# Performance work log

Measured on AMD Instinct MI355X. Metric: run time of the kernel, lower is better.

## Reference

```python
import jax, jax.numpy as jnp
import numpy as np

N = 100000
E = 1600000
D_IN, D_HID, D_OUT = 128, 128, 128


def gcn_conv(x, edge_index, W, b):
    """PyG GCNConv with default symmetric normalization and added self-loops.
    out = D^{-1/2} (A + I) D^{-1/2} (x W) + b, edge weights = 1.
    """
    n = x.shape[0]
    h = x @ W                                   # [N, D_out]
    src, dst = edge_index[0], edge_index[1]     # messages flow src -> dst
    ones = jnp.ones(src.shape[0], dtype=x.dtype)
    # degree includes the self-loop (+1), computed on the target index as in PyG
    deg = jax.ops.segment_sum(ones, dst, num_segments=n) + 1.0  # [N]
    dinv = jax.lax.rsqrt(deg)                   # deg >= 1 so safe
    norm = dinv[src] * dinv[dst]                # [E]
    msg = h[src] * norm[:, None]                # [E, D_out]
    agg = jax.ops.segment_sum(msg, dst, num_segments=n)
    # self-loop contribution: norm = dinv_i * dinv_i = 1/deg_i
    out = agg + h * (dinv * dinv)[:, None] + b
    return out


def layer_norm(x, gamma, beta, eps=1e-5):
    mu = jnp.mean(x, axis=-1, keepdims=True)
    var = jnp.mean(jnp.square(x - mu), axis=-1, keepdims=True)
    return (x - mu) * jax.lax.rsqrt(var + eps) * gamma + beta


def setup_inputs() -> dict:
    key = jax.random.key(0)
    ks = jax.random.split(key, 8)
    x = jax.random.normal(ks[0], (N, D_IN), dtype=jnp.float32)
    edge_index = jax.random.randint(ks[1], (2, E), 0, N, dtype=jnp.int64)
    s1 = 1.0 / np.sqrt(D_IN)
    s2 = 1.0 / np.sqrt(D_HID)
    W1 = jax.random.uniform(ks[2], (D_IN, D_HID), jnp.float32, -s1, s1)
    b1 = jnp.zeros((D_HID,), jnp.float32)
    W2 = jax.random.uniform(ks[3], (D_HID, D_OUT), jnp.float32, -s2, s2)
    b2 = jnp.zeros((D_OUT,), jnp.float32)
    gamma = jnp.ones((D_OUT,), jnp.float32)
    beta = jnp.zeros((D_OUT,), jnp.float32)
    return {"x": x, "edge_index": edge_index, "W1": W1, "b1": b1,
            "W2": W2, "b2": b2, "gamma": gamma, "beta": beta}


def reference(x, edge_index, W1, b1, W2, b2, gamma, beta):
    h = gcn_conv(x, edge_index, W1, b1)
    h = jax.nn.relu(h)
    # dropout is identity in eval mode (deterministic reference)
    h = gcn_conv(h, edge_index, W2, b2)
    return layer_norm(h, gamma, beta)
```

## Files before the change

kernel.cpp:

```cpp
#include <hip/hip_runtime.h>


#define N_NODES 100000
#define N_EDGES 1600000
#define NBLK_N  391
#define NB      196
#define BKT_CAP 8960
#define BIN_GRID 391
#define GEMM_GRID 1563

typedef unsigned int  u32;
typedef unsigned short u16;
typedef __attribute__((ext_vector_type(8))) short bf16x8;
typedef __attribute__((ext_vector_type(4))) float f32x4;

__device__ __forceinline__ float bflo(u32 u){ return __uint_as_float(u << 16); }
__device__ __forceinline__ float bfhi(u32 u){ return __uint_as_float(u & 0xFFFF0000u); }
__device__ __forceinline__ u32 f2b(float f){
  u32 u = __float_as_uint(f);
  return (u + 0x7FFFu + ((u >> 16) & 1u)) >> 16;
}
__device__ __forceinline__ u32 pack2(float a, float b){ return f2b(a) | (f2b(b) << 16); }
__device__ __forceinline__ u32 clampN(int s){
  u32 u = (u32)s;
  return (u < (u32)N_NODES) ? u : (u32)(N_NODES - 1);
}

__global__ __launch_bounds__(64) void detect(const int* __restrict__ ei,
                                             int* __restrict__ flags){
  int l = threadIdx.x;
  int nzodd = (ei[2 * l + 1] != 0) ? 1 : 0;
  #pragma unroll
  for (int o = 32; o > 0; o >>= 1) nzodd += __shfl_xor(nzodd, o, 64);
  if (l == 0) flags[1] = (nzodd == 0) ? 1 : 0;
}


__device__ __forceinline__ void build_wfrag(u16* wfrag, const float* __restrict__ W,
                                            int tid){
  #pragma unroll
  for (int i = 0; i < 8; ++i){
    int fid   = tid + i * 256;
    int lane  = fid & 63;
    int kb    = (fid >> 6) & 3;
    int ntile = fid >> 8;
    int n  = ntile * 16 + (lane & 15);
    int k0 = kb * 32 + (lane >> 4) * 8;
    u16 tmp[8];
    #pragma unroll
    for (int j = 0; j < 8; ++j) tmp[j] = (u16)f2b(W[(k0 + j) * 128 + n]);
    *(bf16x8*)(wfrag + (size_t)fid * 8) = *(const bf16x8*)tmp;
  }
}

__device__ __forceinline__ void gemm_tail(const u16* wfrag, const bf16x8 afrag[4],
                                          int rowbase, int lane, u16* __restrict__ Hout,
                                          int nrows){
  const int m = lane & 15, q = lane >> 4;
  f32x4 acc[8];
  #pragma unroll
  for (int n = 0; n < 8; ++n) acc[n] = (f32x4){0.f, 0.f, 0.f, 0.f};
  #pragma unroll
  for (int n = 0; n < 8; ++n){
    #pragma unroll
    for (int kb = 0; kb < 4; ++kb){
      bf16x8 bfrag = *(const bf16x8*)(wfrag + ((size_t)(n * 4 + kb) * 64 + lane) * 8);
      acc[n] = __builtin_amdgcn_mfma_f32_16x16x32_bf16(afrag[kb], bfrag, acc[n], 0, 0, 0);
    }
  }
  #pragma unroll
  for (int r = 0; r < 4; ++r){
    int orow = rowbase + q * 4 + r;
    if (orow < nrows){
      u16* Or = Hout + (size_t)orow * 128 + m;
      #pragma unroll
      for (int n = 0; n < 8; ++n) Or[n * 16] = (u16)f2b(acc[n][r]);
    }
  }
}

__device__ __forceinline__ void gemm_f32_body(u16* wfrag, const float* __restrict__ A,
                                              const float* __restrict__ W,
                                              u16* __restrict__ Hout, int nrows, int bid){
  build_wfrag(wfrag, W, threadIdx.x);
  __syncthreads();
  const int lane = threadIdx.x & 63;
  const int wv   = threadIdx.x >> 6;
  const int rowbase = bid * 64 + wv * 16;
  const int row  = rowbase + (lane & 15);
  const int rowc = (row < nrows) ? row : (nrows - 1);
  const int q    = lane >> 4;
  bf16x8 afrag[4];
  const float* Ar = A + (size_t)rowc * 128;
  #pragma unroll
  for (int kb = 0; kb < 4; ++kb){
    f32x4 p0 = *(const f32x4*)(Ar + kb * 32 + q * 8);
    f32x4 p1 = *(const f32x4*)(Ar + kb * 32 + q * 8 + 4);
    bf16x8 f;
    f[0] = (short)f2b(p0[0]); f[1] = (short)f2b(p0[1]);
    f[2] = (short)f2b(p0[2]); f[3] = (short)f2b(p0[3]);
    f[4] = (short)f2b(p1[0]); f[5] = (short)f2b(p1[1]);
    f[6] = (short)f2b(p1[2]); f[7] = (short)f2b(p1[3]);
    afrag[kb] = f;
  }
  gemm_tail(wfrag, afrag, rowbase, lane, Hout, nrows);
}

__device__ __forceinline__ void gemm_bf16_body(u16* wfrag, const u16* __restrict__ A,
                                               const float* __restrict__ W,
                                               u16* __restrict__ Hout, int nrows, int bid){
  build_wfrag(wfrag, W, threadIdx.x);
  __syncthreads();
  const int lane = threadIdx.x & 63;
  const int wv   = threadIdx.x >> 6;
  const int rowbase = bid * 64 + wv * 16;
  const int row  = rowbase + (lane & 15);
  const int rowc = (row < nrows) ? row : (nrows - 1);
  const int q    = lane >> 4;
  bf16x8 afrag[4];
  const u16* Ar = A + (size_t)rowc * 128;
  #pragma unroll
  for (int kb = 0; kb < 4; ++kb)
    afrag[kb] = *(const bf16x8*)(Ar + kb * 32 + q * 8);
  gemm_tail(wfrag, afrag, rowbase, lane, Hout, nrows);
}


__device__ __forceinline__ void binA_body(u32* cnt ,
                                          const int* __restrict__ ei,
                                          const int* __restrict__ flags,
                                          u32* __restrict__ binned,
                                          u32* __restrict__ bucket_fill, int bb){
  u32* gbase = cnt + 256;
  const int tid = threadIdx.x;
  cnt[tid] = 0;
  __syncthreads();
  const int i64  = flags[1];
  const int base = bb * 4096;
  u32 pk[16], rk[16], bk[16];
  #pragma unroll
  for (int j = 0; j < 16; ++j){
    int e = base + tid + j * 256;
    bk[j] = 0xFFFFFFFFu;
    if (e < N_EDGES){
      int dsti = i64 ? ei[2 * N_EDGES + 2 * e] : ei[N_EDGES + e];
      int srci = i64 ? ei[2 * e]               : ei[e];
      u32 ud = clampN(dsti), us = clampN(srci);
      u32 b = ud >> 9;
      bk[j] = b;
      pk[j] = us | ((ud & 511u) << 17);
      rk[j] = atomicAdd(&cnt[b], 1u);
    }
  }
  __syncthreads();
  u32 c = cnt[tid];
  u32 old = 0;
  if (c) old = atomicAdd(&bucket_fill[tid < NB ? tid : 0], tid < NB ? c : 0u);
  gbase[tid] = old;
  __syncthreads();
  #pragma unroll
  for (int j = 0; j < 16; ++j){
    if (bk[j] != 0xFFFFFFFFu){
      u32 idx = gbase[bk[j]] + rk[j];
      if (idx < BKT_CAP) binned[(size_t)bk[j] * BKT_CAP + idx] = pk[j];
    }
  }
}


__global__ __launch_bounds__(256) void fused_gemm_bin(const float* __restrict__ A,
                                                      const float* __restrict__ W,
                                                      u16* __restrict__ Hout,
                                                      const int* __restrict__ ei,
                                                      const int* __restrict__ flags,
                                                      u32* __restrict__ binned,
                                                      u32* __restrict__ bucket_fill){
  __shared__ u16 smem[16384];
  if (blockIdx.x < GEMM_GRID){
    gemm_f32_body(smem, A, W, Hout, N_NODES, blockIdx.x);
  } else {
    binA_body((u32*)smem, ei, flags, binned, bucket_fill, blockIdx.x - GEMM_GRID);
  }
}

__global__ __launch_bounds__(256) void gemm_f32in(const float* __restrict__ A,
                                                  const float* __restrict__ W,
                                                  u16* __restrict__ Hout){
  __shared__ u16 smem[16384];
  gemm_f32_body(smem, A, W, Hout, N_NODES, blockIdx.x);
}
__global__ __launch_bounds__(256) void gemm_bf16in(const u16* __restrict__ A,
                                                   const float* __restrict__ W,
                                                   u16* __restrict__ Hout){
  __shared__ u16 smem[16384];
  gemm_bf16_body(smem, A, W, Hout, N_NODES, blockIdx.x);
}


__global__ __launch_bounds__(256) void deg_local(const u32* __restrict__ binned,
                                                 const u32* __restrict__ bucket_fill,
                                                 int* __restrict__ deg){
  const int b = blockIdx.x;
  u32 n = bucket_fill[b]; if (n > BKT_CAP) n = BKT_CAP;
  const u32 basenode = (u32)b << 9;
  for (u32 i = threadIdx.x; i < n; i += 256){
    u32 pk = binned[(size_t)b * BKT_CAP + i];
    u32 dst = basenode + (pk >> 17);
    if (dst < (u32)N_NODES) atomicAdd(&deg[dst], 1);
  }
}

__global__ __launch_bounds__(256) void fill2(const u32* __restrict__ binned,
                                             const u32* __restrict__ bucket_fill,
                                             int* __restrict__ woff,
                                             int* __restrict__ srclist){
  const int b = blockIdx.x;
  u32 n = bucket_fill[b]; if (n > BKT_CAP) n = BKT_CAP;
  const u32 basenode = (u32)b << 9;
  for (u32 i = threadIdx.x; i < n; i += 256){
    u32 pk = binned[(size_t)b * BKT_CAP + i];
    u32 dst = basenode + (pk >> 17);
    if (dst < (u32)N_NODES){
      int p = atomicAdd(&woff[dst], 1);
      if ((unsigned)p < (unsigned)N_EDGES) srclist[p] = (int)(pk & 0x1FFFFu);
    }
  }
}


__global__ __launch_bounds__(256) void count_deg(const int* __restrict__ ei,
                                                 const int* __restrict__ flags,
                                                 int* __restrict__ deg){
  int e   = blockIdx.x * 256 + threadIdx.x;
  int i64 = flags[1];
  int dst = i64 ? ei[2 * N_EDGES + 2 * e] : ei[N_EDGES + e];
  if ((unsigned)dst < (unsigned)N_NODES) atomicAdd(&deg[dst], 1);
}

__global__ __launch_bounds__(256) void fill_edges(const int* __restrict__ ei,
                                                  const int* __restrict__ flags,
                                                  int* __restrict__ woff,
                                                  int* __restrict__ srclist){
  int e   = blockIdx.x * 256 + threadIdx.x;
  int i64 = flags[1];
  int dst = i64 ? ei[2 * N_EDGES + 2 * e] : ei[N_EDGES + e];
  int src = i64 ? ei[2 * e]               : ei[e];
  if ((unsigned)dst < (unsigned)N_NODES){
    int p = atomicAdd(&woff[dst], 1);
    if ((unsigned)p < (unsigned)N_EDGES) srclist[p] = src;
  }
}


__global__ __launch_bounds__(256) void scan1(const int* __restrict__ deg,
                                             int* __restrict__ offs,
                                             int* __restrict__ bsum,
                                             float* __restrict__ dinv){
  __shared__ int sh[256];
  int t = threadIdx.x;
  int i = blockIdx.x * 256 + t;
  int v = (i < N_NODES) ? deg[i] : 0;
  if (i < N_NODES) dinv[i] = rsqrtf((float)v + 1.0f);
  sh[t] = v;
  __syncthreads();
  for (int o = 1; o < 256; o <<= 1){
    int add = (t >= o) ? sh[t - o] : 0;
    __syncthreads();
    sh[t] += add;
    __syncthreads();
  }
  if (i < N_NODES) offs[i] = sh[t] - v;
  if (t == 255)    bsum[blockIdx.x] = sh[255];
}

__global__ __launch_bounds__(512) void scan2(const int* __restrict__ bsum,
                                             int* __restrict__ bofs){
  __shared__ int sh[512];
  int t = threadIdx.x;
  int v = (t < NBLK_N) ? bsum[t] : 0;
  sh[t] = v;
  __syncthreads();
  for (int o = 1; o < 512; o <<= 1){
    int add = (t >= o) ? sh[t - o] : 0;
    __syncthreads();
    sh[t] += add;
    __syncthreads();
  }
  if (t < NBLK_N) bofs[t] = sh[t] - v;
}

__global__ __launch_bounds__(256) void finalize_offs(int* __restrict__ offs,
                                                     const int* __restrict__ bofs,
                                                     int* __restrict__ woff){
  int i = blockIdx.x * 256 + threadIdx.x;
  if (i < N_NODES){
    int o = offs[i] + bofs[blockIdx.x];
    offs[i] = o;
    woff[i] = o;
  }
  if (i == 0) offs[N_NODES] = N_EDGES;
}


#define GATHER_EDGE(sv, A0, A1)                         \
  { u32 s_ = clampN(sv);                                \
    float w_ = dinv[s_];                                \
    u32 h_ = H[s_ * 64 + lane];                         \
    A0 = fmaf(w_, bflo(h_), A0);                        \
    A1 = fmaf(w_, bfhi(h_), A1); }

__global__ __launch_bounds__(256) void gather_relu(const int* __restrict__ offs,
                                                   const int* __restrict__ srcl,
                                                   const u32* __restrict__ H,
                                                   const float* __restrict__ dinv,
                                                   const float* __restrict__ bias,
                                                   u32* __restrict__ X2){
  const int node = blockIdx.x * 4 + (threadIdx.x >> 6);
  const int lane = threadIdx.x & 63;
  int beg = offs[node], end = offs[node + 1];
  if (end > N_EDGES) end = N_EDGES;
  if (beg < 0 || beg > end) beg = end;
  float a0 = 0.f, a1 = 0.f, c0 = 0.f, c1 = 0.f;
  int e = beg;
  for (; e + 8 <= end; e += 8){
    int s0=srcl[e],s1=srcl[e+1],s2=srcl[e+2],s3=srcl[e+3];
    int s4=srcl[e+4],s5=srcl[e+5],s6=srcl[e+6],s7=srcl[e+7];
    GATHER_EDGE(s0,a0,a1) GATHER_EDGE(s1,c0,c1)
    GATHER_EDGE(s2,a0,a1) GATHER_EDGE(s3,c0,c1)
    GATHER_EDGE(s4,a0,a1) GATHER_EDGE(s5,c0,c1)
    GATHER_EDGE(s6,a0,a1) GATHER_EDGE(s7,c0,c1)
  }
  for (; e + 4 <= end; e += 4){
    int s0=srcl[e],s1=srcl[e+1],s2=srcl[e+2],s3=srcl[e+3];
    GATHER_EDGE(s0,a0,a1) GATHER_EDGE(s1,c0,c1)
    GATHER_EDGE(s2,a0,a1) GATHER_EDGE(s3,c0,c1)
  }
  for (; e < end; ++e){ int s0=srcl[e]; GATHER_EDGE(s0,a0,a1) }
  a0 += c0;  a1 += c1;
  float di = dinv[node];
  u32 hs = H[(u32)node * 64 + lane];
  float b0 = bias[2 * lane], b1v = bias[2 * lane + 1];
  float v0 = fmaf(a0, di, fmaf(bflo(hs), di * di, b0));
  float v1 = fmaf(a1, di, fmaf(bfhi(hs), di * di, b1v));
  X2[(u32)node * 64 + lane] = pack2(fmaxf(v0, 0.f), fmaxf(v1, 0.f));
}

__global__ __launch_bounds__(256) void gather_ln(const int* __restrict__ offs,
                                                 const int* __restrict__ srcl,
                                                 const u32* __restrict__ H,
                                                 const float* __restrict__ dinv,
                                                 const float* __restrict__ bias,
                                                 const float* __restrict__ gamma,
                                                 const float* __restrict__ beta,
                                                 float* __restrict__ out){
  const int node = blockIdx.x * 4 + (threadIdx.x >> 6);
  const int lane = threadIdx.x & 63;
  int beg = offs[node], end = offs[node + 1];
  if (end > N_EDGES) end = N_EDGES;
  if (beg < 0 || beg > end) beg = end;
  float a0 = 0.f, a1 = 0.f, c0 = 0.f, c1 = 0.f;
  int e = beg;
  for (; e + 8 <= end; e += 8){
    int s0=srcl[e],s1=srcl[e+1],s2=srcl[e+2],s3=srcl[e+3];
    int s4=srcl[e+4],s5=srcl[e+5],s6=srcl[e+6],s7=srcl[e+7];
    GATHER_EDGE(s0,a0,a1) GATHER_EDGE(s1,c0,c1)
    GATHER_EDGE(s2,a0,a1) GATHER_EDGE(s3,c0,c1)
    GATHER_EDGE(s4,a0,a1) GATHER_EDGE(s5,c0,c1)
    GATHER_EDGE(s6,a0,a1) GATHER_EDGE(s7,c0,c1)
  }
  for (; e + 4 <= end; e += 4){
    int s0=srcl[e],s1=srcl[e+1],s2=srcl[e+2],s3=srcl[e+3];
    GATHER_EDGE(s0,a0,a1) GATHER_EDGE(s1,c0,c1)
    GATHER_EDGE(s2,a0,a1) GATHER_EDGE(s3,c0,c1)
  }
  for (; e < end; ++e){ int s0=srcl[e]; GATHER_EDGE(s0,a0,a1) }
  a0 += c0;  a1 += c1;
  float di = dinv[node];
  u32 hs = H[(u32)node * 64 + lane];
  float b0 = bias[2 * lane], b1v = bias[2 * lane + 1];
  float v0 = fmaf(a0, di, fmaf(bflo(hs), di * di, b0));
  float v1 = fmaf(a1, di, fmaf(bfhi(hs), di * di, b1v));

  float s2 = v0 + v1;
  #pragma unroll
  for (int o = 32; o > 0; o >>= 1) s2 += __shfl_xor(s2, o, 64);
  float mu = s2 * 0.0078125f;
  float d0 = v0 - mu, d1 = v1 - mu;
  float qq = d0 * d0 + d1 * d1;
  #pragma unroll
  for (int o = 32; o > 0; o >>= 1) qq += __shfl_xor(qq, o, 64);
  float rr = rsqrtf(qq * 0.0078125f + 1e-5f);

  float g0 = gamma[2 * lane], g1 = gamma[2 * lane + 1];
  float t0 = beta[2 * lane],  t1 = beta[2 * lane + 1];
  *(float2*)(out + (size_t)node * 128 + 2 * lane) =
      make_float2(fmaf(d0 * rr, g0, t0), fmaf(d1 * rr, g1, t1));
}


extern "C" void kernel_launch(void* const* d_in, const int* in_sizes, int n_in,
                              void* d_out, int out_size, void* d_ws, size_t ws_size,
                              hipStream_t stream){
  const float* x  = (const float*)d_in[0];
  const int*   ei = (const int*)d_in[1];
  const float* W1 = (const float*)d_in[2];
  const float* b1 = (const float*)d_in[3];
  const float* W2 = (const float*)d_in[4];
  const float* b2 = (const float*)d_in[5];
  const float* gm = (const float*)d_in[6];
  const float* bt = (const float*)d_in[7];

  char* ws = (char*)d_ws;
  size_t off = 0;
  auto carve = [&](size_t bytes) -> void* {
    void* p = ws + off;
    off = (off + bytes + 255) & ~(size_t)255;
    return p;
  };
  int*   flags   = (int*)  carve(64);
  int*   offs    = (int*)  carve((size_t)(N_NODES + 1) * 4);
  float* dinv    = (float*)carve((size_t)N_NODES * 4);
  int*   bsum    = (int*)  carve(2048);
  int*   bofs    = (int*)  carve(2048);
  int*   srclist = (int*)  carve((size_t)N_EDGES * 4);
  int*   deg         = (int*)carve((size_t)N_NODES * 4);
  u32*   bucket_fill = (u32*)carve(NB * 4);
  size_t zspan = (size_t)((char*)bucket_fill - (char*)deg) + NB * 4;

  size_t bin_bytes = (size_t)NB * BKT_CAP * 4;
  u32* binned = (u32*)carve(bin_bytes);
  bool use_binned = (ws_size >= off);
  if (!use_binned) off = (size_t)((char*)binned - ws);

  size_t h_bytes = (size_t)N_NODES * 128 * 2;
  u32* H1 = (u32*)d_out;
  u32* X2 = (u32*)d_out + 6400000;
  u32* H2 = (ws_size >= off + h_bytes) ? (u32*)carve(h_bytes) : (u32*)d_in[0];

  hipMemsetAsync(deg, 0, zspan, stream);
  detect<<<1, 64, 0, stream>>>(ei, flags);

  if (use_binned){
    fused_gemm_bin<<<GEMM_GRID + BIN_GRID, 256, 0, stream>>>(x, W1, (u16*)H1, ei, flags,
                                                             binned, bucket_fill);
    deg_local     <<<NB,     256, 0, stream>>>(binned, bucket_fill, deg);
    scan1         <<<NBLK_N, 256, 0, stream>>>(deg, offs, bsum, dinv);
    scan2         <<<1,      512, 0, stream>>>(bsum, bofs);
    finalize_offs <<<NBLK_N, 256, 0, stream>>>(offs, bofs, deg );
    fill2         <<<NB,     256, 0, stream>>>(binned, bucket_fill, deg , srclist);
  } else {
    count_deg     <<<N_EDGES / 256, 256, 0, stream>>>(ei, flags, deg);
    scan1         <<<NBLK_N,        256, 0, stream>>>(deg, offs, bsum, dinv);
    scan2         <<<1,             512, 0, stream>>>(bsum, bofs);
    finalize_offs <<<NBLK_N,        256, 0, stream>>>(offs, bofs, deg );
    fill_edges    <<<N_EDGES / 256, 256, 0, stream>>>(ei, flags, deg , srclist);
    gemm_f32in    <<<GEMM_GRID,     256, 0, stream>>>(x, W1, (u16*)H1);
  }

  gather_relu <<<N_NODES / 4, 256, 0, stream>>>(offs, srclist, H1, dinv, b1, X2);
  gemm_bf16in <<<GEMM_GRID,   256, 0, stream>>>((const u16*)X2, W2, (u16*)H2);
  gather_ln   <<<N_NODES / 4, 256, 0, stream>>>(offs, srclist, H2, dinv, b2, gm, bt,
                                                (float*)d_out);
}
```

Baseline: 373.4 us.

## Fuse per-bucket degree count, scan, and CSR fill into one kernel

Replaces the five-kernel binned CSR build (deg_local, scan1, scan2, finalize_offs, fill2) with one per-bucket kernel. It counts destination degrees in shared memory, derives the bucket base from a reduction over earlier bucket fills, scans locally, writes offs and dinv, and scatters sources with shared-memory atomics. The memset is replaced by zeroing bucket_fill inside the detect kernel. This removes several launches and the global atomics on deg, but each block redundantly reduces bucket_fill and only 196 blocks do the work.

```diff
diff --git a/kernel.cpp b/kernel.cpp
--- a/kernel.cpp
+++ b/kernel.cpp
@@ -11,6 +11,7 @@
 
 typedef unsigned int  u32;
 typedef unsigned short u16;
+typedef unsigned char u8;
 typedef __attribute__((ext_vector_type(8))) short bf16x8;
 typedef __attribute__((ext_vector_type(4))) float f32x4;
 
@@ -26,13 +27,17 @@
   return (u < (u32)N_NODES) ? u : (u32)(N_NODES - 1);
 }
 
-__global__ __launch_bounds__(64) void detect(const int* __restrict__ ei,
-                                             int* __restrict__ flags){
-  int l = threadIdx.x;
-  int nzodd = (ei[2 * l + 1] != 0) ? 1 : 0;
-  #pragma unroll
-  for (int o = 32; o > 0; o >>= 1) nzodd += __shfl_xor(nzodd, o, 64);
-  if (l == 0) flags[1] = (nzodd == 0) ? 1 : 0;
+__global__ __launch_bounds__(256) void detect_init(const int* __restrict__ ei,
+                                                   int* __restrict__ flags,
+                                                   u32* __restrict__ bucket_fill){
+  int t = threadIdx.x;
+  if (t < NB) bucket_fill[t] = 0;
+  if (t < 64){
+    int nzodd = (ei[2 * t + 1] != 0) ? 1 : 0;
+    #pragma unroll
+    for (int o = 32; o > 0; o >>= 1) nzodd += __shfl_xor(nzodd, o, 64);
+    if (t == 0) flags[1] = (nzodd == 0) ? 1 : 0;
+  }
 }
 
 
@@ -54,8 +59,8 @@
 }
 
 __device__ __forceinline__ void gemm_tail(const u16* wfrag, const bf16x8 afrag[4],
-                                          int rowbase, int lane, u16* __restrict__ Hout,
-                                          int nrows){
+                                          int rowbase, int lane,
+                                          u16* __restrict__ Hout, int nrows){
   const int m = lane & 15, q = lane >> 4;
   f32x4 acc[8];
   #pragma unroll
@@ -197,33 +202,73 @@
 }
 
 
-__global__ __launch_bounds__(256) void deg_local(const u32* __restrict__ binned,
+__global__ __launch_bounds__(256) void fill_sort(const u32* __restrict__ binned,
                                                  const u32* __restrict__ bucket_fill,
-                                                 int* __restrict__ deg){
-  const int b = blockIdx.x;
+                                                 int* __restrict__ offs,
+                                                 float* __restrict__ dinv,
+                                                 int* __restrict__ srclist){
+  __shared__ u32 cnt[512];
+  __shared__ u32 sc[512];
+  __shared__ u32 red[256];
+  const int b   = blockIdx.x;
+  const int tid = threadIdx.x;
+  cnt[tid] = 0; cnt[tid + 256] = 0;
+  __syncthreads();
+
   u32 n = bucket_fill[b]; if (n > BKT_CAP) n = BKT_CAP;
+  const u32* eb = binned + (size_t)b * BKT_CAP;
+
+  for (u32 i = tid; i < n; i += 256)
+    atomicAdd(&cnt[eb[i] >> 17], 1u);
+
+  u32 v = 0;
+  if (tid < b && tid < NB){
+    u32 f = bucket_fill[tid];
+    v = (f > BKT_CAP) ? BKT_CAP : f;
+  }
+  red[tid] = v;
+  __syncthreads();
+  for (int o = 128; o > 0; o >>= 1){
+    if (tid < o) red[tid] += red[tid + o];
+    __syncthreads();
+  }
+  const u32 base = red[0];
+  __syncthreads();
+
+  u32 pair = cnt[2 * tid] + cnt[2 * tid + 1];
+  red[tid] = pair;
+  __syncthreads();
+  for (int o = 1; o < 256; o <<= 1){
+    u32 add = (tid >= o) ? red[tid - o] : 0;
+    __syncthreads();
+    red[tid] += add;
+    __syncthreads();
+  }
+  u32 pex = red[tid] - pair;
+  sc[2 * tid]     = pex;
+  sc[2 * tid + 1] = pex + cnt[2 * tid];
+  __syncthreads();
+
   const u32 basenode = (u32)b << 9;
-  for (u32 i = threadIdx.x; i < n; i += 256){
-    u32 pk = binned[(size_t)b * BKT_CAP + i];
-    u32 dst = basenode + (pk >> 17);
-    if (dst < (u32)N_NODES) atomicAdd(&deg[dst], 1);
-  }
-}
-
-__global__ __launch_bounds__(256) void fill2(const u32* __restrict__ binned,
-                                             const u32* __restrict__ bucket_fill,
-                                             int* __restrict__ woff,
-                                             int* __restrict__ srclist){
-  const int b = blockIdx.x;
-  u32 n = bucket_fill[b]; if (n > BKT_CAP) n = BKT_CAP;
-  const u32 basenode = (u32)b << 9;
-  for (u32 i = threadIdx.x; i < n; i += 256){
-    u32 pk = binned[(size_t)b * BKT_CAP + i];
-    u32 dst = basenode + (pk >> 17);
-    if (dst < (u32)N_NODES){
-      int p = atomicAdd(&woff[dst], 1);
-      if ((unsigned)p < (unsigned)N_EDGES) srclist[p] = (int)(pk & 0x1FFFFu);
+  #pragma unroll
+  for (int h = 0; h < 2; ++h){
+    u32 l = tid + h * 256;
+    u32 node = basenode + l;
+    if (node < (u32)N_NODES){
+      offs[node] = (int)(base + sc[l]);
+      dinv[node] = rsqrtf((float)cnt[l] + 1.0f);
     }
+  }
+  if (b == NB - 1 && tid == 0) offs[N_NODES] = (int)(base + n);
+
+  __syncthreads();
+  cnt[tid] = 0; cnt[tid + 256] = 0;
+  __syncthreads();
+  for (u32 i = tid; i < n; i += 256){
+    u32 pk = eb[i];
+    u32 d  = pk >> 17;
+    u32 r  = atomicAdd(&cnt[d], 1u);
+    srclist[base + sc[d] + r] = (int)(pk & 0x1FFFFu);
   }
 }
 
@@ -250,7 +295,6 @@
     if ((unsigned)p < (unsigned)N_EDGES) srclist[p] = src;
   }
 }
-
 
 __global__ __launch_bounds__(256) void scan1(const int* __restrict__ deg,
                                              int* __restrict__ offs,
@@ -417,15 +461,14 @@
     off = (off + bytes + 255) & ~(size_t)255;
     return p;
   };
-  int*   flags   = (int*)  carve(64);
-  int*   offs    = (int*)  carve((size_t)(N_NODES + 1) * 4);
-  float* dinv    = (float*)carve((size_t)N_NODES * 4);
-  int*   bsum    = (int*)  carve(2048);
-  int*   bofs    = (int*)  carve(2048);
-  int*   srclist = (int*)  carve((size_t)N_EDGES * 4);
-  int*   deg         = (int*)carve((size_t)N_NODES * 4);
-  u32*   bucket_fill = (u32*)carve(NB * 4);
-  size_t zspan = (size_t)((char*)bucket_fill - (char*)deg) + NB * 4;
+  int*   flags       = (int*)  carve(64);
+  u32*   bucket_fill = (u32*)  carve(NB * 4);
+  int*   offs        = (int*)  carve((size_t)(N_NODES + 1) * 4);
+  float* dinv        = (float*)carve((size_t)N_NODES * 4);
+  int*   srclist     = (int*)  carve((size_t)N_EDGES * 4);
+  int*   deg         = (int*)  carve((size_t)N_NODES * 4);
+  int*   bsum        = (int*)  carve(2048);
+  int*   bofs        = (int*)  carve(2048);
 
   size_t bin_bytes = (size_t)NB * BKT_CAP * 4;
   u32* binned = (u32*)carve(bin_bytes);
@@ -437,18 +480,14 @@
   u32* X2 = (u32*)d_out + 6400000;
   u32* H2 = (ws_size >= off + h_bytes) ? (u32*)carve(h_bytes) : (u32*)d_in[0];
 
-  hipMemsetAsync(deg, 0, zspan, stream);
-  detect<<<1, 64, 0, stream>>>(ei, flags);
+  detect_init<<<1, 256, 0, stream>>>(ei, flags, bucket_fill);
 
   if (use_binned){
     fused_gemm_bin<<<GEMM_GRID + BIN_GRID, 256, 0, stream>>>(x, W1, (u16*)H1, ei, flags,
                                                              binned, bucket_fill);
-    deg_local     <<<NB,     256, 0, stream>>>(binned, bucket_fill, deg);
-    scan1         <<<NBLK_N, 256, 0, stream>>>(deg, offs, bsum, dinv);
-    scan2         <<<1,      512, 0, stream>>>(bsum, bofs);
-    finalize_offs <<<NBLK_N, 256, 0, stream>>>(offs, bofs, deg );
-    fill2         <<<NB,     256, 0, stream>>>(binned, bucket_fill, deg , srclist);
+    fill_sort     <<<NB, 256, 0, stream>>>(binned, bucket_fill, offs, dinv, srclist);
   } else {
+    hipMemsetAsync(deg, 0, (size_t)N_NODES * 4, stream);
     count_deg     <<<N_EDGES / 256, 256, 0, stream>>>(ei, flags, deg);
     scan1         <<<NBLK_N,        256, 0, stream>>>(deg, offs, bsum, dinv);
     scan2         <<<1,             512, 0, stream>>>(bsum, bofs);
```

Result: faster. 313.8 us (-16.0%).
